# Performance work log

Measured on AMD Instinct MI355X. Metric: run time of the kernel, lower is better.

The kernel has to match this reference:

```python
import jax, jax.numpy as jnp
import numpy as np

N = 50000      # nodes
E = 800000     # edges (avg degree 16)
IN = 128
H = 128
OUT = 1000
K = 10
EPS = 1e-5


def setup_inputs() -> dict:
    key = jax.random.key(0)
    ks = jax.random.split(key, 12)
    s = 0.05  # small init scale for weights
    return {
        "x": jax.random.normal(ks[0], (N, IN), jnp.float32),
        "edge_index": jax.random.randint(ks[1], (2, E), 0, N, dtype=jnp.int32),
        "W1": jax.random.normal(ks[2], (IN, H), jnp.float32) * s,
        "b1": jnp.zeros((H,), jnp.float32),
        "g1": jnp.ones((H,), jnp.float32),
        "be1": jnp.zeros((H,), jnp.float32),
        "W2": jax.random.normal(ks[3], (H, H), jnp.float32) * s,
        "b2": jnp.zeros((H,), jnp.float32),
        "g2": jnp.ones((H,), jnp.float32),
        "be2": jnp.zeros((H,), jnp.float32),
        "att": jax.random.uniform(ks[4], (K + 1,), jnp.float32),  # uniform_(0,1) init
        "W3": jax.random.normal(ks[5], (H, H // 2), jnp.float32) * s,
        "b3": jnp.zeros((H // 2,), jnp.float32),
        "g3": jnp.ones((H // 2,), jnp.float32),
        "be3": jnp.zeros((H // 2,), jnp.float32),
        "Wout": jax.random.normal(ks[6], (H // 2, OUT), jnp.float32) * s,
        "bout": jnp.zeros((OUT,), jnp.float32),
    }


def _bn(x, g, b):
    # training-mode BatchNorm1d: biased batch stats over the node dim
    m = jnp.mean(x, axis=0)
    v = jnp.var(x, axis=0)
    return g * (x - m) * jax.lax.rsqrt(v + EPS) + b


def reference(x, edge_index, W1, b1, g1, be1, W2, b2, g2, be2, att,
              W3, b3, g3, be3, Wout, bout):
    # input MLP with residual
    h = jax.nn.relu(_bn(x @ W1 + b1, g1, be1))
    identity = h
    h = jax.nn.relu(_bn(h @ W2 + b2, g2, be2)) + identity

    # DAGNN: K unnormalized scatter-add hops (APPNP.propagate with edge_weight=1),
    # then softmax(att)-weighted sum over hop representations. Accumulate the
    # weighted sum on the fly instead of materializing the [N, H, K+1] stack.
    src, dst = edge_index[0], edge_index[1]  # message flows src -> dst
    w = jax.nn.softmax(att)
    out = w[0] * h
    cur = h
    for i in range(K):
        cur = jax.ops.segment_sum(cur[src], dst, num_segments=N)
        out = out + w[i + 1] * cur

    # output MLP
    h3 = jax.nn.relu(_bn(out @ W3 + b3, g3, be3))
    return h3 @ Wout + bout
```

## Files before the change

kernel.cpp:

```cpp
#include <hip/hip_runtime.h>
#include <cstdint>
#include <cstddef>

#define N_NODES 50000
#define N_EDGES 800000
#define DIM_H   128
#define DIM_P   64
#define DIM_OUT 1000
#define OUT_PAD 1024
#define KHOPS   10
#define BN_EPS  1e-5f

static inline int ceil_div(int a, int b) { return (a + b - 1) / b; }

typedef short  bf16x8  __attribute__((ext_vector_type(8)));
typedef float  floatx4 __attribute__((ext_vector_type(4)));

__device__ __forceinline__ unsigned short f2bf_rne(float v) {
    unsigned int u = __float_as_uint(v);
    return (unsigned short)((u + 0x7fffu + ((u >> 16) & 1u)) >> 16);
}
__device__ __forceinline__ float bf2f(unsigned short u) {
    return __uint_as_float((unsigned int)u << 16);
}

__global__ void init_all(const float* __restrict__ att, float* __restrict__ w,
                         const float* __restrict__ Wout, unsigned short* __restrict__ WT,
                         double* __restrict__ st, int* __restrict__ deg) {
    const int gid = blockIdx.x * blockDim.x + threadIdx.x;
    const int stride = gridDim.x * blockDim.x;
    if (gid == 0) {
        float mx = att[0];
        for (int i = 1; i < KHOPS + 1; ++i) mx = fmaxf(mx, att[i]);
        float e[KHOPS + 1];
        float s = 0.f;
        for (int i = 0; i < KHOPS + 1; ++i) { e[i] = expf(att[i] - mx); s += e[i]; }
        for (int i = 0; i < KHOPS + 1; ++i) w[i] = e[i] / s;
    }
    for (int i = gid; i < 640; i += stride) st[i] = 0.0;
    for (int i = gid; i < N_NODES; i += stride) deg[i] = 0;
    for (int i = gid; i < OUT_PAD * DIM_P; i += stride) {
        int c = i >> 6, k = i & 63;
        WT[i] = (c < DIM_OUT) ? f2bf_rne(Wout[(size_t)k * DIM_OUT + c]) : (unsigned short)0;
    }
}

__global__ void count_deg(const int* __restrict__ dst, int* __restrict__ deg, int ne) {
    int i = blockIdx.x * blockDim.x + threadIdx.x;
    if (i < ne) atomicAdd(&deg[dst[i]], 1);
}

__global__ __launch_bounds__(1024) void scan_local(const int* __restrict__ deg,
                                                   int* __restrict__ row_ptr,
                                                   int* __restrict__ bsums, int n) {
    __shared__ int wsum[16];
    const int i = blockIdx.x * 1024 + threadIdx.x;
    const int lane = threadIdx.x & 63, w = threadIdx.x >> 6;
    int v = (i < n) ? deg[i] : 0;
    int s = v;
#pragma unroll
    for (int d = 1; d < 64; d <<= 1) {
        int t = __shfl_up(s, d, 64);
        if (lane >= d) s += t;
    }
    if (lane == 63) wsum[w] = s;
    __syncthreads();
    if (w == 0) {
        int x = (lane < 16) ? wsum[lane] : 0;
#pragma unroll
        for (int d = 1; d < 16; d <<= 1) {
            int t = __shfl_up(x, d, 64);
            if (lane >= d) x += t;
        }
        if (lane < 16) wsum[lane] = x;
    }
    __syncthreads();
    int incl = s + ((w > 0) ? wsum[w - 1] : 0);
    if (i < n) row_ptr[i + 1] = incl;
    if (threadIdx.x == 1023) bsums[blockIdx.x] = incl;
}

__global__ void scan_finish(int* __restrict__ row_ptr, int* __restrict__ deg,
                            const int* __restrict__ bsums, int n, int nb) {
    __shared__ int boff[64];
    if (threadIdx.x < 64) {
        int lane = threadIdx.x;
        int v = (lane < nb) ? bsums[lane] : 0;
        int s = v;
#pragma unroll
        for (int d = 1; d < 64; d <<= 1) {
            int t = __shfl_up(s, d, 64);
            if (lane >= d) s += t;
        }
        boff[lane] = s - v;
    }
    __syncthreads();
    int i = blockIdx.x * blockDim.x + threadIdx.x;
    if (i < n) {
        int incl = row_ptr[i + 1] + boff[i >> 10];
        row_ptr[i + 1] = incl;
        deg[i] = incl - deg[i];
    }
    if (i == 0) row_ptr[0] = 0;
}

__global__ void fill_csr(const int* __restrict__ src, const int* __restrict__ dst,
                         int* __restrict__ cursor, int* __restrict__ col, int ne) {
    int i = blockIdx.x * blockDim.x + threadIdx.x;
    if (i < ne) {
        int d = dst[i];
        int pos = atomicAdd(&cursor[d], 1);
        col[pos] = src[i];
    }
}

template<int KD, int CPB, bool STATS, bool OBF>
__global__ __launch_bounds__(256) void gemm_fused(
    const float* __restrict__ A,  const double* __restrict__ stA,
    const float* __restrict__ gA, const float* __restrict__ beA,
    const float* __restrict__ A2, const double* __restrict__ stA2,
    const float* __restrict__ gA2, const float* __restrict__ beA2,
    const float* __restrict__ W,
    float* __restrict__ C, float* __restrict__ C2, const float* __restrict__ w0p,
    double* __restrict__ stOut, int n, int M) {
    constexpr int CG  = CPB / 4;
    constexpr int RG  = 256 / CG;
    constexpr int RPT = 64 / RG;
    __shared__ float As[64][KD + 4];
    __shared__ float scA_l[2][KD];
    __shared__ float scA2_l[2][KD];

    const int tid  = threadIdx.x;
    const int cg   = tid % CG;
    const int rg   = tid / CG;
    const int row0 = blockIdx.x * 64;
    const int col0 = blockIdx.y * CPB + cg * 4;

    if (stA && tid < KD) {
        double m = stA[tid] / n;
        double v = stA[KD + tid] / n - m * m;
        float scale = gA[tid] * rsqrtf((float)v + BN_EPS);
        scA_l[0][tid] = scale;
        scA_l[1][tid] = beA[tid] - (float)m * scale;
    }
    if (A2 && tid < KD) {
        double m = stA2[tid] / n;
        double v = stA2[KD + tid] / n - m * m;
        float scale = gA2[tid] * rsqrtf((float)v + BN_EPS);
        scA2_l[0][tid] = scale;
        scA2_l[1][tid] = beA2[tid] - (float)m * scale;
    }
    if (stA || A2) __syncthreads();

    constexpr int VECS = 64 * KD / 4;
    for (int i = tid; i < VECS; i += 256) {
        int r  = i / (KD / 4);
        int k4 = (i % (KD / 4)) * 4;
        float4 v = make_float4(0.f, 0.f, 0.f, 0.f);
        int row = row0 + r;
        if (row < n) {
            v = *reinterpret_cast<const float4*>(A + (size_t)row * KD + k4);
            if (stA) {
                float4 sc = *reinterpret_cast<const float4*>(&scA_l[0][k4]);
                float4 sh = *reinterpret_cast<const float4*>(&scA_l[1][k4]);
                v.x = fmaxf(v.x * sc.x + sh.x, 0.f);
                v.y = fmaxf(v.y * sc.y + sh.y, 0.f);
                v.z = fmaxf(v.z * sc.z + sh.z, 0.f);
                v.w = fmaxf(v.w * sc.w + sh.w, 0.f);
            }
            if (A2) {
                float4 u  = *reinterpret_cast<const float4*>(A2 + (size_t)row * KD + k4);
                float4 sc = *reinterpret_cast<const float4*>(&scA2_l[0][k4]);
                float4 sh = *reinterpret_cast<const float4*>(&scA2_l[1][k4]);
                v.x += fmaxf(u.x * sc.x + sh.x, 0.f);
                v.y += fmaxf(u.y * sc.y + sh.y, 0.f);
                v.z += fmaxf(u.z * sc.z + sh.z, 0.f);
                v.w += fmaxf(u.w * sc.w + sh.w, 0.f);
            }
        }
        *reinterpret_cast<float4*>(&As[r][k4]) = v;
    }
    __syncthreads();

    float acc[RPT][4];
#pragma unroll
    for (int r = 0; r < RPT; ++r)
#pragma unroll
        for (int c = 0; c < 4; ++c) acc[r][c] = 0.f;

    if (col0 < M) {
        for (int k4 = 0; k4 < KD; k4 += 4) {
            float4 w0 = *reinterpret_cast<const float4*>(W + (size_t)(k4 + 0) * M + col0);
            float4 w1 = *reinterpret_cast<const float4*>(W + (size_t)(k4 + 1) * M + col0);
            float4 w2 = *reinterpret_cast<const float4*>(W + (size_t)(k4 + 2) * M + col0);
            float4 w3 = *reinterpret_cast<const float4*>(W + (size_t)(k4 + 3) * M + col0);
#pragma unroll
            for (int r = 0; r < RPT; ++r) {
                float4 a = *reinterpret_cast<const float4*>(&As[rg * RPT + r][k4]);
                acc[r][0] += a.x * w0.x + a.y * w1.x + a.z * w2.x + a.w * w3.x;
                acc[r][1] += a.x * w0.y + a.y * w1.y + a.z * w2.y + a.w * w3.y;
                acc[r][2] += a.x * w0.z + a.y * w1.z + a.z * w2.z + a.w * w3.z;
                acc[r][3] += a.x * w0.w + a.y * w1.w + a.z * w2.w + a.w * w3.w;
            }
        }

        const float w0s = C2 ? w0p[0] : 0.f;
#pragma unroll
        for (int r = 0; r < RPT; ++r) {
            int row = row0 + rg * RPT + r;
            if (row < n) {
                float4 o = make_float4(acc[r][0], acc[r][1], acc[r][2], acc[r][3]);
                if (OBF) {
                    unsigned short* cb = reinterpret_cast<unsigned short*>(C);
                    ushort4 p;
                    p.x = f2bf_rne(o.x); p.y = f2bf_rne(o.y);
                    p.z = f2bf_rne(o.z); p.w = f2bf_rne(o.w);
                    *reinterpret_cast<ushort4*>(cb + (size_t)row * M + col0) = p;
                } else {
                    *reinterpret_cast<float4*>(C + (size_t)row * M + col0) = o;
                }
                if (C2) {
                    float4 q = make_float4(w0s * o.x, w0s * o.y, w0s * o.z, w0s * o.w);
                    *reinterpret_cast<float4*>(C2 + (size_t)row * M + col0) = q;
                }
            }
        }
    }

    if (STATS) {
        float s[4] = {0.f, 0.f, 0.f, 0.f}, q[4] = {0.f, 0.f, 0.f, 0.f};
#pragma unroll
        for (int r = 0; r < RPT; ++r) {
            int row = row0 + rg * RPT + r;
            if (row < n) {
#pragma unroll
                for (int c = 0; c < 4; ++c) {
                    float v = acc[r][c];
                    s[c] += v;
                    q[c] += v * v;
                }
            }
        }
        __syncthreads();
        float* sb = &As[0][0];
        float* qb = sb + RG * CPB;
#pragma unroll
        for (int c = 0; c < 4; ++c) {
            sb[rg * CPB + cg * 4 + c] = s[c];
            qb[rg * CPB + cg * 4 + c] = q[c];
        }
        __syncthreads();
        if (rg == 0 && col0 < M) {
#pragma unroll
            for (int c = 0; c < 4; ++c) {
                float ts = 0.f, tq = 0.f;
#pragma unroll
                for (int g2 = 0; g2 < RG; ++g2) {
                    ts += sb[g2 * CPB + cg * 4 + c];
                    tq += qb[g2 * CPB + cg * 4 + c];
                }
                atomicAdd(&stOut[col0 + c], (double)ts);
                atomicAdd(&stOut[M + col0 + c], (double)tq);
            }
        }
    }
}

template<int M>
__global__ __launch_bounds__(256) void colstats(const float* __restrict__ Z,
                                                double* __restrict__ st, int n) {
    constexpr int RG = 256 / M;
    const int tid = threadIdx.x;
    const int c = tid % M, rg = tid / M;
    double s = 0.0, ss = 0.0;
    for (int row = blockIdx.x * RG + rg; row < n; row += gridDim.x * RG) {
        float v = Z[(size_t)row * M + c];
        s += v;
        ss += (double)v * (double)v;
    }
    __shared__ double sh[2][256];
    sh[0][tid] = s;
    sh[1][tid] = ss;
    __syncthreads();
    if (rg == 0) {
#pragma unroll
        for (int g = 1; g < RG; ++g) { s += sh[0][c + g * M]; ss += sh[1][c + g * M]; }
        atomicAdd(&st[c], s);
        atomicAdd(&st[M + c], ss);
    }
}

__global__ __launch_bounds__(256) void propagate(
    const unsigned short* __restrict__ cur, unsigned short* __restrict__ nxt,
    float* __restrict__ oacc,
    const int* __restrict__ row_ptr, const int* __restrict__ col,
    const float* __restrict__ wts, int hop, int n) {
    const int node = blockIdx.x * 4 + (threadIdx.x >> 6);
    const int lane = threadIdx.x & 63;
    const int g = lane >> 3;
    const int l = lane & 7;
    if (node >= n) return;
    const int beg = row_ptr[node], end = row_ptr[node + 1];
    float acc[8];
#pragma unroll
    for (int j = 0; j < 8; ++j) acc[j] = 0.f;

    int e = beg;
    for (; e + 16 <= end; e += 16) {
        int s0 = col[e + g];
        int s1 = col[e + g + 8];
        bf16x8 v0 = *reinterpret_cast<const bf16x8*>(cur + (size_t)s0 * DIM_P + l * 8);
        bf16x8 v1 = *reinterpret_cast<const bf16x8*>(cur + (size_t)s1 * DIM_P + l * 8);
#pragma unroll
        for (int j = 0; j < 8; ++j)
            acc[j] += bf2f((unsigned short)v0[j]) + bf2f((unsigned short)v1[j]);
    }
    if (e + 8 <= end) {
        int s = col[e + g];
        bf16x8 v = *reinterpret_cast<const bf16x8*>(cur + (size_t)s * DIM_P + l * 8);
#pragma unroll
        for (int j = 0; j < 8; ++j) acc[j] += bf2f((unsigned short)v[j]);
        e += 8;
    }
    if (e + g < end) {
        int s = col[e + g];
        bf16x8 v = *reinterpret_cast<const bf16x8*>(cur + (size_t)s * DIM_P + l * 8);
#pragma unroll
        for (int j = 0; j < 8; ++j) acc[j] += bf2f((unsigned short)v[j]);
    }

#pragma unroll
    for (int off = 8; off < 64; off <<= 1) {
#pragma unroll
        for (int j = 0; j < 8; ++j) acc[j] += __shfl_xor(acc[j], off, 64);
    }

    if (g == 0) {
        const size_t o = (size_t)node * DIM_P + l * 8;
        if (nxt) {
            bf16x8 ov;
#pragma unroll
            for (int j = 0; j < 8; ++j) ov[j] = (short)f2bf_rne(acc[j]);
            *reinterpret_cast<bf16x8*>(nxt + o) = ov;
        }
        const float w = wts[hop];
        float* op = oacc + o;
        float4 t0 = *reinterpret_cast<const float4*>(op);
        float4 t1 = *reinterpret_cast<const float4*>(op + 4);
        t0.x = fmaf(w, acc[0], t0.x); t0.y = fmaf(w, acc[1], t0.y);
        t0.z = fmaf(w, acc[2], t0.z); t0.w = fmaf(w, acc[3], t0.w);
        t1.x = fmaf(w, acc[4], t1.x); t1.y = fmaf(w, acc[5], t1.y);
        t1.z = fmaf(w, acc[6], t1.z); t1.w = fmaf(w, acc[7], t1.w);
        *reinterpret_cast<float4*>(op) = t0;
        *reinterpret_cast<float4*>(op + 4) = t1;
    }
}

__global__ void bn3_relu_bf16(const float* __restrict__ Z, const double* __restrict__ st3,
                              const float* __restrict__ g3, const float* __restrict__ be3,
                              unsigned short* __restrict__ O) {
    __shared__ float sc[DIM_P], sh[DIM_P];
    if (threadIdx.x < DIM_P) {
        int c = threadIdx.x;
        double m = st3[c] / N_NODES;
        double v = st3[DIM_P + c] / N_NODES - m * m;
        float scale = g3[c] * rsqrtf((float)v + BN_EPS);
        sc[c] = scale;
        sh[c] = be3[c] - (float)m * scale;
    }
    __syncthreads();
    const int total8 = N_NODES * DIM_P / 8;
    int i = blockIdx.x * blockDim.x + threadIdx.x;
    if (i >= total8) return;
    int base = i * 8;
    int c = base & (DIM_P - 1);
    float4 z0 = *reinterpret_cast<const float4*>(Z + base);
    float4 z1 = *reinterpret_cast<const float4*>(Z + base + 4);
    float4 s0 = *reinterpret_cast<const float4*>(&sc[c]);
    float4 s1 = *reinterpret_cast<const float4*>(&sc[c + 4]);
    float4 h0 = *reinterpret_cast<const float4*>(&sh[c]);
    float4 h1 = *reinterpret_cast<const float4*>(&sh[c + 4]);
    bf16x8 o;
    o[0] = (short)f2bf_rne(fmaxf(z0.x * s0.x + h0.x, 0.f));
    o[1] = (short)f2bf_rne(fmaxf(z0.y * s0.y + h0.y, 0.f));
    o[2] = (short)f2bf_rne(fmaxf(z0.z * s0.z + h0.z, 0.f));
    o[3] = (short)f2bf_rne(fmaxf(z0.w * s0.w + h0.w, 0.f));
    o[4] = (short)f2bf_rne(fmaxf(z1.x * s1.x + h1.x, 0.f));
    o[5] = (short)f2bf_rne(fmaxf(z1.y * s1.y + h1.y, 0.f));
    o[6] = (short)f2bf_rne(fmaxf(z1.z * s1.z + h1.z, 0.f));
    o[7] = (short)f2bf_rne(fmaxf(z1.w * s1.w + h1.w, 0.f));
    *reinterpret_cast<bf16x8*>(O + base) = o;
}

__global__ __launch_bounds__(256, 4) void out_gemm_mfma(
    const unsigned short* __restrict__ ABF, const unsigned short* __restrict__ WT,
    const float* __restrict__ bout, float* __restrict__ out) {
    const int wave = threadIdx.x >> 6;
    const int lane = threadIdx.x & 63;
    const int m    = lane & 15;
    const int quad = lane >> 4;
    const int kb   = quad * 8;
    const int c0   = blockIdx.y * 256 + wave * 64;

    bf16x8 afrag[4][2];
    float4 bias[4];
#pragma unroll
    for (int t = 0; t < 4; ++t) {
        const unsigned short* wrow = WT + (size_t)(c0 + t * 16 + m) * DIM_P;
        afrag[t][0] = *reinterpret_cast<const bf16x8*>(wrow + kb);
        afrag[t][1] = *reinterpret_cast<const bf16x8*>(wrow + 32 + kb);
        int cc = c0 + t * 16 + quad * 4;
        bias[t] = (cc < DIM_OUT) ? *reinterpret_cast<const float4*>(bout + cc)
                                 : make_float4(0.f, 0.f, 0.f, 0.f);
    }

    const int NT = N_NODES / 16;
    for (int rt = blockIdx.x; rt < NT; rt += gridDim.x) {
        const int row = rt * 16 + m;
        const unsigned short* arow = ABF + (size_t)row * DIM_P;
        bf16x8 bfrag0 = *reinterpret_cast<const bf16x8*>(arow + kb);
        bf16x8 bfrag1 = *reinterpret_cast<const bf16x8*>(arow + 32 + kb);
        float* orow = out + (size_t)row * DIM_OUT;
#pragma unroll
        for (int t = 0; t < 4; ++t) {
            floatx4 acc = {0.f, 0.f, 0.f, 0.f};
            acc = __builtin_amdgcn_mfma_f32_16x16x32_bf16(afrag[t][0], bfrag0, acc, 0, 0, 0);
            acc = __builtin_amdgcn_mfma_f32_16x16x32_bf16(afrag[t][1], bfrag1, acc, 0, 0, 0);
            int cc = c0 + t * 16 + quad * 4;
            if (cc < DIM_OUT) {
                float4 o = make_float4(acc[0] + bias[t].x, acc[1] + bias[t].y,
                                       acc[2] + bias[t].z, acc[3] + bias[t].w);
                *reinterpret_cast<float4*>(orow + cc) = o;
            }
        }
    }
}

extern "C" void kernel_launch(void* const* d_in, const int* in_sizes, int n_in,
                              void* d_out, int out_size, void* d_ws, size_t ws_size,
                              hipStream_t stream) {
    const float* x    = (const float*)d_in[0];
    const int*   ei   = (const int*)  d_in[1];
    const float* W1   = (const float*)d_in[2];
    const float* g1   = (const float*)d_in[4];
    const float* be1  = (const float*)d_in[5];
    const float* W2   = (const float*)d_in[6];
    const float* g2   = (const float*)d_in[8];
    const float* be2  = (const float*)d_in[9];
    const float* att  = (const float*)d_in[10];
    const float* W3   = (const float*)d_in[11];
    const float* g3   = (const float*)d_in[13];
    const float* be3  = (const float*)d_in[14];
    const float* Wout = (const float*)d_in[15];
    const float* bout = (const float*)d_in[16];
    float* out = (float*)d_out;

    char* base = (char*)d_ws;
    size_t off = 0;
    auto alloc = [&](size_t bytes) -> void* {
        void* r = base + off;
        off += (bytes + 255) & ~(size_t)255;
        return r;
    };
    float*  f0      = (float*) alloc((size_t)N_NODES * DIM_H * 4);
    float*  f1      = (float*) alloc((size_t)N_NODES * DIM_H * 4);
    unsigned short* yb = (unsigned short*)alloc((size_t)N_NODES * DIM_P * 2);
    unsigned short* tb = (unsigned short*)alloc((size_t)N_NODES * DIM_P * 2);
    float*  oa      = (float*) alloc((size_t)N_NODES * DIM_P * 4);
    double* st      = (double*)alloc(640 * 8);
    float*  wts     = (float*) alloc(16 * 4);
    int*    row_ptr = (int*)   alloc((size_t)(N_NODES + 1) * 4);
    int*    deg     = (int*)   alloc((size_t)N_NODES * 4);
    int*    col     = (int*)   alloc((size_t)N_EDGES * 4);
    int*    bsums   = (int*)   alloc(64 * 4);
    unsigned short* WT  = (unsigned short*)alloc((size_t)OUT_PAD * DIM_P * 2);
    unsigned short* ABF = (unsigned short*)alloc((size_t)N_NODES * DIM_P * 2);

    const int* src = ei;
    const int* dst = ei + N_EDGES;
    double* st1 = st;   double* st2 = st + 256; double* st3 = st + 512;

    init_all<<<256, 256, 0, stream>>>(att, wts, Wout, WT, st, deg);

    count_deg<<<ceil_div(N_EDGES, 256), 256, 0, stream>>>(dst, deg, N_EDGES);
    const int NB = ceil_div(N_NODES, 1024);
    scan_local<<<NB, 1024, 0, stream>>>(deg, row_ptr, bsums, N_NODES);
    scan_finish<<<ceil_div(N_NODES, 256), 256, 0, stream>>>(row_ptr, deg, bsums,
                                                            N_NODES, NB);
    fill_csr<<<ceil_div(N_EDGES, 256), 256, 0, stream>>>(src, dst, deg, col, N_EDGES);

    const int RB = ceil_div(N_NODES, 64);

    gemm_fused<128, 128, true, false><<<dim3(RB, 1), 256, 0, stream>>>(
        x, nullptr, nullptr, nullptr,
        nullptr, nullptr, nullptr, nullptr,
        W1, f0, nullptr, nullptr, st1, N_NODES, DIM_H);

    gemm_fused<128, 128, true, false><<<dim3(RB, 1), 256, 0, stream>>>(
        f0, st1, g1, be1,
        nullptr, nullptr, nullptr, nullptr,
        W2, f1, nullptr, nullptr, st2, N_NODES, DIM_H);

    gemm_fused<128, 64, false, true><<<dim3(RB, 1), 256, 0, stream>>>(
        f1, st2, g2, be2,
        f0, st1, g1, be1,
        W3, (float*)yb, oa, wts, nullptr, N_NODES, DIM_P);

    {
        unsigned short* cur = yb;
        unsigned short* nxt = tb;
        for (int hop = 1; hop <= KHOPS; ++hop) {
            propagate<<<ceil_div(N_NODES, 4), 256, 0, stream>>>(
                cur, (hop == KHOPS) ? nullptr : nxt, oa, row_ptr, col, wts, hop, N_NODES);
            unsigned short* t = cur; cur = nxt; nxt = t;
        }
    }

    colstats<64><<<256, 256, 0, stream>>>(oa, st3, N_NODES);
    bn3_relu_bf16<<<ceil_div(N_NODES * DIM_P / 8, 256), 256, 0, stream>>>(
        oa, st3, g3, be3, ABF);

    out_gemm_mfma<<<dim3(512, 4), 256, 0, stream>>>(ABF, WT, bout, out);
}
```

Baseline: 872.6 us.

## Store all hop outputs in bf16 and compute weighted sum plus stats at end

```diff
diff --git a/kernel.cpp b/kernel.cpp
--- a/kernel.cpp
+++ b/kernel.cpp
@@ -114,15 +114,14 @@
     }
 }
 
-template<int KD, int CPB, bool STATS, bool OBF>
+template<int KD, int CPB, bool OBF>
 __global__ __launch_bounds__(256) void gemm_fused(
     const float* __restrict__ A,  const double* __restrict__ stA,
     const float* __restrict__ gA, const float* __restrict__ beA,
     const float* __restrict__ A2, const double* __restrict__ stA2,
     const float* __restrict__ gA2, const float* __restrict__ beA2,
     const float* __restrict__ W,
-    float* __restrict__ C, float* __restrict__ C2, const float* __restrict__ w0p,
-    double* __restrict__ stOut, int n, int M) {
+    float* __restrict__ C, int n, int M) {
     constexpr int CG  = CPB / 4;
     constexpr int RG  = 256 / CG;
     constexpr int RPT = 64 / RG;
@@ -182,85 +181,42 @@
     }
     __syncthreads();
 
+    if (col0 >= M) return;
+
     float acc[RPT][4];
 #pragma unroll
     for (int r = 0; r < RPT; ++r)
 #pragma unroll
         for (int c = 0; c < 4; ++c) acc[r][c] = 0.f;
 
-    if (col0 < M) {
-        for (int k4 = 0; k4 < KD; k4 += 4) {
-            float4 w0 = *reinterpret_cast<const float4*>(W + (size_t)(k4 + 0) * M + col0);
-            float4 w1 = *reinterpret_cast<const float4*>(W + (size_t)(k4 + 1) * M + col0);
-            float4 w2 = *reinterpret_cast<const float4*>(W + (size_t)(k4 + 2) * M + col0);
-            float4 w3 = *reinterpret_cast<const float4*>(W + (size_t)(k4 + 3) * M + col0);
-#pragma unroll
-            for (int r = 0; r < RPT; ++r) {
-                float4 a = *reinterpret_cast<const float4*>(&As[rg * RPT + r][k4]);
-                acc[r][0] += a.x * w0.x + a.y * w1.x + a.z * w2.x + a.w * w3.x;
-                acc[r][1] += a.x * w0.y + a.y * w1.y + a.z * w2.y + a.w * w3.y;
-                acc[r][2] += a.x * w0.z + a.y * w1.z + a.z * w2.z + a.w * w3.z;
-                acc[r][3] += a.x * w0.w + a.y * w1.w + a.z * w2.w + a.w * w3.w;
-            }
-        }
-
-        const float w0s = C2 ? w0p[0] : 0.f;
+    for (int k4 = 0; k4 < KD; k4 += 4) {
+        float4 w0 = *reinterpret_cast<const float4*>(W + (size_t)(k4 + 0) * M + col0);
+        float4 w1 = *reinterpret_cast<const float4*>(W + (size_t)(k4 + 1) * M + col0);
+        float4 w2 = *reinterpret_cast<const float4*>(W + (size_t)(k4 + 2) * M + col0);
+        float4 w3 = *reinterpret_cast<const float4*>(W + (size_t)(k4 + 3) * M + col0);
 #pragma unroll
         for (int r = 0; r < RPT; ++r) {
-            int row = row0 + rg * RPT + r;
-            if (row < n) {
-                float4 o = make_float4(acc[r][0], acc[r][1], acc[r][2], acc[r][3]);
-                if (OBF) {
-                    unsigned short* cb = reinterpret_cast<unsigned short*>(C);
-                    ushort4 p;
-                    p.x = f2bf_rne(o.x); p.y = f2bf_rne(o.y);
-                    p.z = f2bf_rne(o.z); p.w = f2bf_rne(o.w);
-                    *reinterpret_cast<ushort4*>(cb + (size_t)row * M + col0) = p;
-                } else {
-                    *reinterpret_cast<float4*>(C + (size_t)row * M + col0) = o;
-                }
-                if (C2) {
-                    float4 q = make_float4(w0s * o.x, w0s * o.y, w0s * o.z, w0s * o.w);
-                    *reinterpret_cast<float4*>(C2 + (size_t)row * M + col0) = q;
-                }
-            }
-        }
-    }
-
-    if (STATS) {
-        float s[4] = {0.f, 0.f, 0.f, 0.f}, q[4] = {0.f, 0.f, 0.f, 0.f};
-#pragma unroll
-        for (int r = 0; r < RPT; ++r) {
-            int row = row0 + rg * RPT + r;
-            if (row < n) {
-#pragma unroll
-                for (int c = 0; c < 4; ++c) {
-                    float v = acc[r][c];
-                    s[c] += v;
-                    q[c] += v * v;
-                }
-            }
-        }
-        __syncthreads();
-        float* sb = &As[0][0];
-        float* qb = sb + RG * CPB;
-#pragma unroll
-        for (int c = 0; c < 4; ++c) {
-            sb[rg * CPB + cg * 4 + c] = s[c];
-            qb[rg * CPB + cg * 4 + c] = q[c];
-        }
-        __syncthreads();
-        if (rg == 0 && col0 < M) {
-#pragma unroll
-            for (int c = 0; c < 4; ++c) {
-                float ts = 0.f, tq = 0.f;
-#pragma unroll
-                for (int g2 = 0; g2 < RG; ++g2) {
-                    ts += sb[g2 * CPB + cg * 4 + c];
-                    tq += qb[g2 * CPB + cg * 4 + c];
-                }
-                atomicAdd(&stOut[col0 + c], (double)ts);
-                atomicAdd(&stOut[M + col0 + c], (double)tq);
+            float4 a = *reinterpret_cast<const float4*>(&As[rg * RPT + r][k4]);
+            acc[r][0] += a.x * w0.x + a.y * w1.x + a.z * w2.x + a.w * w3.x;
+            acc[r][1] += a.x * w0.y + a.y * w1.y + a.z * w2.y + a.w * w3.y;
+            acc[r][2] += a.x * w0.z + a.y * w1.z + a.z * w2.z + a.w * w3.z;
+            acc[r][3] += a.x * w0.w + a.y * w1.w + a.z * w2.w + a.w * w3.w;
+        }
+    }
+
+#pragma unroll
+    for (int r = 0; r < RPT; ++r) {
+        int row = row0 + rg * RPT + r;
+        if (row < n) {
+            float4 o = make_float4(acc[r][0], acc[r][1], acc[r][2], acc[r][3]);
+            if (OBF) {
+                unsigned short* cb = reinterpret_cast<unsigned short*>(C);
+                ushort4 p;
+                p.x = f2bf_rne(o.x); p.y = f2bf_rne(o.y);
+                p.z = f2bf_rne(o.z); p.w = f2bf_rne(o.w);
+                *reinterpret_cast<ushort4*>(cb + (size_t)row * M + col0) = p;
+            } else {
+                *reinterpret_cast<float4*>(C + (size_t)row * M + col0) = o;
             }
         }
     }
@@ -292,9 +248,7 @@
 
 __global__ __launch_bounds__(256) void propagate(
     const unsigned short* __restrict__ cur, unsigned short* __restrict__ nxt,
-    float* __restrict__ oacc,
-    const int* __restrict__ row_ptr, const int* __restrict__ col,
-    const float* __restrict__ wts, int hop, int n) {
+    const int* __restrict__ row_ptr, const int* __restrict__ col, int n) {
     const int node = blockIdx.x * 4 + (threadIdx.x >> 6);
     const int lane = threadIdx.x & 63;
     const int g = lane >> 3;
@@ -336,23 +290,42 @@
     }
 
     if (g == 0) {
-        const size_t o = (size_t)node * DIM_P + l * 8;
-        if (nxt) {
-            bf16x8 ov;
-#pragma unroll
-            for (int j = 0; j < 8; ++j) ov[j] = (short)f2bf_rne(acc[j]);
-            *reinterpret_cast<bf16x8*>(nxt + o) = ov;
-        }
-        const float w = wts[hop];
-        float* op = oacc + o;
-        float4 t0 = *reinterpret_cast<const float4*>(op);
-        float4 t1 = *reinterpret_cast<const float4*>(op + 4);
-        t0.x = fmaf(w, acc[0], t0.x); t0.y = fmaf(w, acc[1], t0.y);
-        t0.z = fmaf(w, acc[2], t0.z); t0.w = fmaf(w, acc[3], t0.w);
-        t1.x = fmaf(w, acc[4], t1.x); t1.y = fmaf(w, acc[5], t1.y);
-        t1.z = fmaf(w, acc[6], t1.z); t1.w = fmaf(w, acc[7], t1.w);
-        *reinterpret_cast<float4*>(op) = t0;
-        *reinterpret_cast<float4*>(op + 4) = t1;
+        bf16x8 ov;
+#pragma unroll
+        for (int j = 0; j < 8; ++j) ov[j] = (short)f2bf_rne(acc[j]);
+        *reinterpret_cast<bf16x8*>(nxt + (size_t)node * DIM_P + l * 8) = ov;
+    }
+}
+
+__global__ __launch_bounds__(256) void wsum_stats(
+    const unsigned short* __restrict__ hs, const float* __restrict__ wts,
+    float* __restrict__ oa, double* __restrict__ st, int n) {
+    const int tid = threadIdx.x;
+    const int c = tid & 63, rg = tid >> 6;
+    float w[KHOPS + 1];
+#pragma unroll
+    for (int i = 0; i < KHOPS + 1; ++i) w[i] = wts[i];
+    const size_t stride = (size_t)n * DIM_P;
+    double s = 0.0, ss = 0.0;
+    for (int row = blockIdx.x * 4 + rg; row < n; row += gridDim.x * 4) {
+        const size_t idx = (size_t)row * DIM_P + c;
+        float val = 0.f;
+#pragma unroll
+        for (int i = 0; i < KHOPS + 1; ++i)
+            val += w[i] * bf2f(hs[idx + (size_t)i * stride]);
+        oa[idx] = val;
+        s += val;
+        ss += (double)val * (double)val;
+    }
+    __shared__ double sh[2][256];
+    sh[0][tid] = s;
+    sh[1][tid] = ss;
+    __syncthreads();
+    if (rg == 0) {
+#pragma unroll
+        for (int g2 = 1; g2 < 4; ++g2) { s += sh[0][c + g2 * 64]; ss += sh[1][c + g2 * 64]; }
+        atomicAdd(&st[c], s);
+        atomicAdd(&st[64 + c], ss);
     }
 }
 
@@ -462,11 +435,11 @@
         off += (bytes + 255) & ~(size_t)255;
         return r;
     };
+    const size_t SSTRIDE = (size_t)N_NODES * DIM_P;
     float*  f0      = (float*) alloc((size_t)N_NODES * DIM_H * 4);
     float*  f1      = (float*) alloc((size_t)N_NODES * DIM_H * 4);
-    unsigned short* yb = (unsigned short*)alloc((size_t)N_NODES * DIM_P * 2);
-    unsigned short* tb = (unsigned short*)alloc((size_t)N_NODES * DIM_P * 2);
-    float*  oa      = (float*) alloc((size_t)N_NODES * DIM_P * 4);
+    unsigned short* hs = (unsigned short*)alloc((size_t)(KHOPS + 1) * SSTRIDE * 2);
+    float*  oa      = (float*) alloc(SSTRIDE * 4);
     double* st      = (double*)alloc(640 * 8);
     float*  wts     = (float*) alloc(16 * 4);
     int*    row_ptr = (int*)   alloc((size_t)(N_NODES + 1) * 4);
@@ -474,7 +447,7 @@
     int*    col     = (int*)   alloc((size_t)N_EDGES * 4);
     int*    bsums   = (int*)   alloc(64 * 4);
     unsigned short* WT  = (unsigned short*)alloc((size_t)OUT_PAD * DIM_P * 2);
-    unsigned short* ABF = (unsigned short*)alloc((size_t)N_NODES * DIM_P * 2);
+    unsigned short* ABF = (unsigned short*)alloc(SSTRIDE * 2);
 
     const int* src = ei;
     const int* dst = ei + N_EDGES;
@@ -491,32 +464,30 @@
 
     const int RB = ceil_div(N_NODES, 64);
 
-    gemm_fused<128, 128, true, false><<<dim3(RB, 1), 256, 0, stream>>>(
+    gemm_fused<128, 128, false><<<dim3(RB, 1), 256, 0, stream>>>(
         x, nullptr, nullptr, nullptr,
         nullptr, nullptr, nullptr, nullptr,
-        W1, f0, nullptr, nullptr, st1, N_NODES, DIM_H);
-
-    gemm_fused<128, 128, true, false><<<dim3(RB, 1), 256, 0, stream>>>(
+        W1, f0, N_NODES, DIM_H);
+    colstats<128><<<256, 256, 0, stream>>>(f0, st1, N_NODES);
+
+    gemm_fused<128, 128, false><<<dim3(RB, 1), 256, 0, stream>>>(
         f0, st1, g1, be1,
         nullptr, nullptr, nullptr, nullptr,
-        W2, f1, nullptr, nullptr, st2, N_NODES, DIM_H);
-
-    gemm_fused<128, 64, false, true><<<dim3(RB, 1), 256, 0, stream>>>(
+        W2, f1, N_NODES, DIM_H);
+    colstats<128><<<256, 256, 0, stream>>>(f1, st2, N_NODES);
+
+    gemm_fused<128, 64, true><<<dim3(RB, 1), 256, 0, stream>>>(
         f1, st2, g2, be2,
         f0, st1, g1, be1,
-        W3, (float*)yb, oa, wts, nullptr, N_NODES, DIM_P);
-
-    {
-        unsigned short* cur = yb;
-        unsigned short* nxt = tb;
-        for (int hop = 1; hop <= KHOPS; ++hop) {
-            propagate<<<ceil_div(N_NODES, 4), 256, 0, stream>>>(
-                cur, (hop == KHOPS) ? nullptr : nxt, oa, row_ptr, col, wts, hop, N_NODES);
-            unsigned short* t = cur; cur = nxt; nxt = t;
-        }
-    }
-
-    colstats<64><<<256, 256, 0, stream>>>(oa, st3, N_NODES);
+        W3, (float*)hs, N_NODES, DIM_P);
+
+    for (int hop = 1; hop <= KHOPS; ++hop) {
+        propagate<<<ceil_div(N_NODES, 4), 256, 0, stream>>>(
+            hs + (size_t)(hop - 1) * SSTRIDE, hs + (size_t)hop * SSTRIDE,
+            row_ptr, col, N_NODES);
+    }
+
+    wsum_stats<<<256, 256, 0, stream>>>(hs, wts, oa, st3, N_NODES);
     bn3_relu_bf16<<<ceil_div(N_NODES * DIM_P / 8, 256), 256, 0, stream>>>(
         oa, st3, g3, be3, ABF);
 
```

Measured after the change: 759.9 us. 12.9% less time.
